# Optimization experiments

Measured on AMD Instinct MI355X. Metric: run time of the kernel, lower is better.

## Reference

```python
import jax, jax.numpy as jnp
import numpy as np
import math

DIM = 1024
CHUNK = 64
B, S = 4, 4096

def setup_inputs() -> dict:
    key = jax.random.key(0)
    ks = jax.random.split(key, 16)
    d = DIM
    std = 1.0 / math.sqrt(d)
    def lin(k):
        k1, k2 = jax.random.split(k)
        return (jax.random.uniform(k1, (d, d), jnp.float32, -std, std),
                jax.random.uniform(k2, (d,), jnp.float32, -std, std))
    Wk, bk = lin(ks[0])
    Wv, bv = lin(ks[1])
    Wq, bq = lin(ks[2])
    Wkp, bkp = lin(ks[3])
    Wqp, bqp = lin(ks[4])
    Wo, bo = lin(ks[5])
    return {
        "x": jax.random.normal(ks[6], (B, S, d), jnp.float32),
        "Wk": Wk, "bk": bk, "Wv": Wv, "bv": bv, "Wq": Wq, "bq": bq,
        "Wkp": Wkp, "bkp": bkp, "Wqp": Wqp, "bqp": bqp,
        "phase_scale": jnp.full((d,), math.pi, jnp.float32),
        "ln_g": jnp.ones((d,), jnp.float32),
        "ln_b": jnp.zeros((d,), jnp.float32),
        "Wo": Wo, "bo": bo,
    }

def _linear(x, W, b):
    # torch nn.Linear: x @ W.T + b
    return jnp.einsum('bsd,ed->bse', x, W) + b

def _layernorm(x, g, b, eps=1e-5):
    mu = jnp.mean(x, axis=-1, keepdims=True)
    var = jnp.var(x, axis=-1, keepdims=True)
    return (x - mu) * jax.lax.rsqrt(var + eps) * g + b

def reference(x, Wk, bk, Wv, bv, Wq, bq, Wkp, bkp, Wqp, bqp,
              phase_scale, ln_g, ln_b, Wo, bo):
    batch, seq_len, dim = x.shape
    key = _linear(x, Wk, bk)
    value = _linear(x, Wv, bv)
    query = _linear(x, Wq, bq)
    key_phase = jnp.tanh(_linear(key, Wkp, bkp)) * phase_scale
    query_phase = jnp.tanh(_linear(query, Wqp, bqp)) * phase_scale
    bound_real = value * jnp.cos(key_phase)
    bound_imag = value * jnpp_sin(key_phase) if False else value * jnp.sin(key_phase)
    pad_len = (CHUNK - seq_len % CHUNK) % CHUNK
    if pad_len > 0:
        pad = ((0, 0), (0, pad_len), (0, 0))
        bound_real = jnp.pad(bound_real, pad)
        bound_imag = jnp.pad(bound_imag, pad)
        query_phase = jnp.pad(query_phase, pad)
    padded_len = bound_real.shape[1]
    nc = padded_len // CHUNK
    br = bound_real.reshape(batch, nc, CHUNK, dim)
    bi = bound_imag.reshape(batch, nc, CHUNK, dim)
    qp = query_phase.reshape(batch, nc, CHUNK, dim)
    mem_real = jnp.cumsum(br, axis=2)
    mem_imag = jnp.cumsum(bi, axis=2)
    retrieved = mem_real * jnp.cos(qp) + mem_imag * jnp.sin(qp)
    retrieved = retrieved.reshape(batch, padded_len, dim)[:, :seq_len]
    retrieved = retrieved / math.sqrt(dim)
    out = _linear(_layernorm(retrieved, ln_g, ln_b), Wo, bo)
    return x + out
```

## Files before the change

kernel.cpp:

```cpp
#include <hip/hip_runtime.h>
#include <math.h>

#define DIMD 1024
#define CHUNKLEN 64
#define NTOK 16384

#define TM 128
#define TN 128
#define BK 64

typedef __bf16 bf16x8 __attribute__((ext_vector_type(8)));
typedef float floatx4 __attribute__((ext_vector_type(4)));
typedef unsigned short ushort8v __attribute__((ext_vector_type(8)));

__device__ __forceinline__ float bf2f(unsigned short u) {
  union { unsigned int i; float f; } v; v.i = ((unsigned int)u) << 16; return v.f;
}
__device__ __forceinline__ unsigned short f2bf(float f) {
  union { float f; unsigned int i; } v; v.f = f;
  unsigned int r = v.i + 0x7FFFu + ((v.i >> 16) & 1u);
  return (unsigned short)(r >> 16);
}

__device__ __forceinline__ float tanh_fast(float v) {
  const float t = __expf(2.0f * v);
  return 1.0f - 2.0f * __builtin_amdgcn_rcpf(t + 1.0f);
}

__device__ __forceinline__ void async16(const unsigned short* g, unsigned short* l) {
  __builtin_amdgcn_global_load_lds(
      (const __attribute__((address_space(1))) unsigned int*)g,
      (__attribute__((address_space(3))) unsigned int*)l, 16, 0, 0);
}

__global__ __launch_bounds__(256) void cvt_all_kernel(
    const float* __restrict__ x,
    const float* __restrict__ w0, const float* __restrict__ w1,
    const float* __restrict__ w2, const float* __restrict__ w3,
    unsigned short* __restrict__ dx,
    unsigned short* __restrict__ d0, unsigned short* __restrict__ d1,
    unsigned short* __restrict__ d2, unsigned short* __restrict__ d3)
{
  const int b = blockIdx.x;
  const float* src; unsigned short* dst; long i;
  if (b < 16384) {
    src = x; dst = dx; i = (long)b * 256 + threadIdx.x;
  } else {
    const int r = b - 16384;
    const int s = r >> 10;
    src = s == 0 ? w0 : s == 1 ? w1 : s == 2 ? w2 : w3;
    dst = s == 0 ? d0 : s == 1 ? d1 : s == 2 ? d2 : d3;
    i = (long)(r & 1023) * 256 + threadIdx.x;
  }
  const float4 v = ((const float4*)src)[i];
  ushort4 o;
  o.x = f2bf(v.x); o.y = f2bf(v.y); o.z = f2bf(v.z); o.w = f2bf(v.w);
  ((ushort4*)dst)[i] = o;
}

__global__ __launch_bounds__(256) void transpose_cvt_kernel(
    const float* __restrict__ s0, const float* __restrict__ s1,
    unsigned short* __restrict__ q0, unsigned short* __restrict__ q1)
{
  __shared__ unsigned short tile[64][66];
  const float* src = blockIdx.z ? s1 : s0;
  unsigned short* dst = blockIdx.z ? q1 : q0;
  const int e0 = blockIdx.y * 64;
  const int k0 = blockIdx.x * 64;
  const int t  = threadIdx.x;
  const int tr = t >> 4;
  const int tc = t & 15;
#pragma unroll
  for (int p = 0; p < 4; ++p) {
    const int el = p * 16 + tr;
    const float4 v = *(const float4*)&src[(long)(e0 + el) * DIMD + k0 + tc * 4];
    tile[el][tc * 4 + 0] = f2bf(v.x);
    tile[el][tc * 4 + 1] = f2bf(v.y);
    tile[el][tc * 4 + 2] = f2bf(v.z);
    tile[el][tc * 4 + 3] = f2bf(v.w);
  }
  __syncthreads();
#pragma unroll
  for (int p = 0; p < 4; ++p) {
    const int kl = p * 16 + tr;
    ushort4 o;
    o.x = tile[tc * 4 + 0][kl];
    o.y = tile[tc * 4 + 1][kl];
    o.z = tile[tc * 4 + 2][kl];
    o.w = tile[tc * 4 + 3][kl];
    *(ushort4*)&dst[(long)(k0 + kl) * DIMD + e0 + tc * 4] = o;
  }
}

__global__ __launch_bounds__(256) void bias_comb_kernel(
    const float* __restrict__ Wkp, const float* __restrict__ bk,
    const float* __restrict__ bkp,
    const float* __restrict__ Wqp, const float* __restrict__ bq,
    const float* __restrict__ bqp,
    float* __restrict__ bkq, float* __restrict__ bqq)
{
  const int b = blockIdx.x;
  const int which = b >> 8;
  const int lane = threadIdx.x & 63;
  const int wid  = threadIdx.x >> 6;
  const int n = (b & 255) * 4 + wid;
  const float* W    = which ? Wqp : Wkp;
  const float* bvec = which ? bq  : bk;
  const float* badd = which ? bqp : bkp;
  float*       outp = which ? bqq : bkq;
  float s = 0.f;
#pragma unroll
  for (int i = 0; i < 16; ++i)
    s += W[(long)n * DIMD + lane + i * 64] * bvec[lane + i * 64];
#pragma unroll
  for (int o = 32; o > 0; o >>= 1) s += __shfl_xor(s, o, 64);
  if (lane == 0) outp[n] = s + badd[n];
}

template <int MODE>
__global__ __launch_bounds__(256) void gemm_bt_kernel(
    const unsigned short* __restrict__ A0, const unsigned short* __restrict__ A1,
    const unsigned short* __restrict__ W0, const unsigned short* __restrict__ W1,
    const unsigned short* __restrict__ W2,
    const float* __restrict__ b0, const float* __restrict__ b1,
    const float* __restrict__ b2,
    const float* __restrict__ aux,
    unsigned short* __restrict__ O0, unsigned short* __restrict__ O1,
    unsigned short* __restrict__ O2,
    float* __restrict__ Of, const float* __restrict__ resid)
{
  __shared__ unsigned short lsA[TM * BK];
  __shared__ unsigned short lsB[TN * BK];

  const int tid  = threadIdx.x;
  const int lane = tid & 63;
  const int wid  = tid >> 6;
  const long bm  = (long)blockIdx.y * TM;
  const long bng = (long)blockIdx.x * TN;

  const unsigned short* A = A0;
  const unsigned short* W = W0;
  const float* bias = b0;
  unsigned short* Ob = O0;
  long bn = bng;
  int seg = 0;
  if (MODE == 0) {
    seg = (int)(bng >> 10);
    bn = bng & 1023;
    W    = seg == 0 ? W0 : (seg == 1 ? W1 : W2);
    bias = seg == 0 ? b0 : (seg == 1 ? b1 : b2);
    Ob   = seg == 0 ? O0 : (seg == 1 ? O1 : O2);
  } else if (MODE == 1) {
    if (blockIdx.z) { A = A1; W = W1; Ob = O1; }
  }

  const int wm = (wid & 1) * 64;
  const int wn = (wid >> 1) * 64;

  floatx4 acc[4][4];
#pragma unroll
  for (int i = 0; i < 4; ++i)
#pragma unroll
    for (int j = 0; j < 4; ++j)
      acc[i][j] = (floatx4)(0.0f);

  const int srow  = lane >> 3;
  const int pcol  = (lane & 7) * 8;
  const int lcolL = (((lane & 7) ^ (srow & 7)) * 8);
  const int frm   = lane & 15;
  const int cfrk  = lane >> 4;

  for (int kk = 0; kk < DIMD; kk += BK) {
    __syncthreads();
#pragma unroll
    for (int j = 0; j < 4; ++j) {
      const int inst = wid * 4 + j;
      const int r = inst * 8 + srow;
      async16(A + (bm + r) * (long)DIMD + kk + lcolL, &lsA[r * BK + pcol]);
      async16(W + (bn + r) * (long)DIMD + kk + lcolL, &lsB[r * BK + pcol]);
    }
    __syncthreads();
#pragma unroll
    for (int ks = 0; ks < BK; ks += 32) {
      const int cb  = (ks >> 3) + cfrk;
      const int swz = ((cb ^ (frm & 7)) << 3);
      bf16x8 af[4], bfr[4];
#pragma unroll
      for (int i = 0; i < 4; ++i)
        af[i]  = *(const bf16x8*)&lsA[(wm + i * 16 + frm) * BK + swz];
#pragma unroll
      for (int i = 0; i < 4; ++i)
        bfr[i] = *(const bf16x8*)&lsB[(wn + i * 16 + frm) * BK + swz];
#pragma unroll
      for (int i = 0; i < 4; ++i)
#pragma unroll
        for (int j = 0; j < 4; ++j)
          acc[i][j] = __builtin_amdgcn_mfma_f32_16x16x32_bf16(af[i], bfr[j], acc[i][j], 0, 0, 0);
    }
  }

  const int cn = lane & 15;
  const int rq = (lane >> 4) * 4;
#pragma unroll
  for (int j = 0; j < 4; ++j) {
    const long col = bn + wn + j * 16 + cn;
    const float bv = (MODE == 1) ? 0.0f : bias[col];
    const float pv = (MODE == 0) ? aux[col] : 0.0f;
#pragma unroll
    for (int i = 0; i < 4; ++i) {
#pragma unroll
      for (int r = 0; r < 4; ++r) {
        const long row = bm + wm + i * 16 + rq + r;
        const float v = acc[i][j][r] + bv;
        if (MODE == 0) {
          Ob[row * (long)DIMD + col] = (seg == 0) ? f2bf(v)
                                                  : f2bf(tanh_fast(v) * pv);
        } else if (MODE == 1) {
          Ob[row * (long)DIMD + col] = f2bf(v);
        } else {
          Of[row * (long)DIMD + col] = v + resid[row * (long)DIMD + col];
        }
      }
    }
  }
}

#define TILE16 16384
#define HALF16 8192

template <int MODE>
__global__ __launch_bounds__(512, 2) void gemm256_kernel(
    const unsigned short* __restrict__ A,
    const unsigned short* __restrict__ W0, const unsigned short* __restrict__ W1,
    const unsigned short* __restrict__ W2,
    const float* __restrict__ b0, const float* __restrict__ b1,
    const float* __restrict__ b2,
    const float* __restrict__ aux,
    unsigned short* __restrict__ O0, unsigned short* __restrict__ O1,
    unsigned short* __restrict__ O2,
    float* __restrict__ Of, const float* __restrict__ resid)
{
  __shared__ unsigned short lds[4 * TILE16];

  const int tid  = threadIdx.x;
  const int lane = tid & 63;
  const int wid  = tid >> 6;

  constexpr int NBX = (MODE == 0) ? 12 : 4;
  constexpr int NWG = NBX * 64;
  const int orig = blockIdx.x + blockIdx.y * gridDim.x;
  const int swzb = (orig & 7) * (NWG >> 3) + (orig >> 3);
  const int nb = swzb % NBX;
  const int mb = swzb / NBX;

  const long bm = (long)mb * 256;
  long bn;
  int seg = 0;
  const unsigned short* W = W0;
  const float* bias = b0;
  unsigned short* Ob = O0;
  if (MODE == 0) {
    seg = nb >> 2;
    bn  = (long)(nb & 3) * 256;
    W    = seg == 0 ? W0 : (seg == 1 ? W1 : W2);
    bias = seg == 0 ? b0 : (seg == 1 ? b1 : b2);
    Ob   = seg == 0 ? O0 : (seg == 1 ? O1 : O2);
  } else {
    bn = (long)nb * 256;
  }

  const int wm = (wid >> 2) * 128;
  const int wn = (wid & 3) * 64;

  const int q0  = wid * 2;
  const int sr0 = q0 * 16 + (lane >> 2);
  const int sg  = (((lane & 3) ^ ((sr0 >> 1) & 3)) * 8);
  const int sd0 = q0 * 512 + lane * 8;
  const long arow = (bm + sr0) * (long)DIMD;
  const long brow = (bn + sr0) * (long)DIMD;

  const int frm   = lane & 15;
  const int cfrk  = lane >> 4;
  const int slot8 = (cfrk ^ ((frm >> 1) & 3)) * 8;
  const int rbase = frm * 32 + slot8;

  floatx4 acc[8][4];
#pragma unroll
  for (int i = 0; i < 8; ++i)
#pragma unroll
    for (int j = 0; j < 4; ++j) acc[i][j] = (floatx4)(0.0f);

  bf16x8 bfr[4];

#define SA256(buf, kk, h) do { \
    const unsigned short* _s = A + arow + (kk) + (h) * 32 + sg; \
    unsigned short* _d = &lds[(buf) * TILE16 + (h) * HALF16 + sd0]; \
    async16(_s, _d); \
    async16(_s + 16 * DIMD, _d + 512); \
  } while (0)
#define SB256(buf, kk, h) do { \
    const unsigned short* _s = W + brow + (kk) + (h) * 32 + sg; \
    unsigned short* _d = &lds[2 * TILE16 + (buf) * TILE16 + (h) * HALF16 + sd0]; \
    async16(_s, _d); \
    async16(_s + 16 * DIMD, _d + 512); \
  } while (0)
#define RDA256(buf, h, ih, af) do { \
    const int _ab = (buf) * TILE16 + (h) * HALF16 + (wm + (ih) * 64) * 32 + rbase; \
    _Pragma("unroll") \
    for (int _i = 0; _i < 4; ++_i) (af)[_i] = *(const bf16x8*)&lds[_ab + _i * 512]; \
  } while (0)
#define RDB256(buf, h) do { \
    const int _bb = 2 * TILE16 + (buf) * TILE16 + (h) * HALF16 + wn * 32 + rbase; \
    _Pragma("unroll") \
    for (int _j = 0; _j < 4; ++_j) bfr[_j] = *(const bf16x8*)&lds[_bb + _j * 512]; \
  } while (0)
#define VMW4() asm volatile("s_waitcnt vmcnt(4)" ::: "memory")
#define BAR256() do { \
    asm volatile("" ::: "memory"); \
    __builtin_amdgcn_s_barrier(); \
    asm volatile("" ::: "memory"); \
  } while (0)
#define MFMA16(ih, af) do { \
    __builtin_amdgcn_s_setprio(1); \
    _Pragma("unroll") \
    for (int _i = 0; _i < 4; ++_i) \
      _Pragma("unroll") \
      for (int _j = 0; _j < 4; ++_j) \
        acc[(ih) * 4 + _i][_j] = __builtin_amdgcn_mfma_f32_16x16x32_bf16( \
            (af)[_i], bfr[_j], acc[(ih) * 4 + _i][_j], 0, 0, 0); \
    __builtin_amdgcn_s_setprio(0); \
  } while (0)
#define KTILE(c, n, kn) do { \
    { bf16x8 af[4]; RDA256(c, 0, 0, af); RDB256(c, 0); \
      SA256(n, kn, 0); MFMA16(0, af); } \
    { bf16x8 af[4]; RDA256(c, 0, 1, af); \
      SB256(n, kn, 0); VMW4(); BAR256(); MFMA16(1, af); } \
    { bf16x8 af[4]; RDA256(c, 1, 0, af); RDB256(c, 1); \
      SA256(n, kn, 1); MFMA16(0, af); } \
    { bf16x8 af[4]; RDA256(c, 1, 1, af); \
      SB256(n, kn, 1); VMW4(); BAR256(); MFMA16(1, af); } \
  } while (0)

  SA256(0, 0, 0); SB256(0, 0, 0); SA256(0, 0, 1); SB256(0, 0, 1);
  VMW4();
  BAR256();

#pragma unroll 1
  for (int t = 0; t < 16; t += 2) {
    const int k1 = (t + 1) * 64;
    const int k2 = (t + 2 < 16) ? (t + 2) * 64 : 0;
    KTILE(0, 1, k1);
    KTILE(1, 0, k2);
  }
  asm volatile("s_waitcnt vmcnt(0)" ::: "memory");

#undef SA256
#undef SB256
#undef RDA256
#undef RDB256
#undef VMW4
#undef BAR256
#undef MFMA16
#undef KTILE

  const int cn = lane & 15;
  const int rq = (lane >> 4) * 4;
  long colj[4]; float bvj[4], pvj[4];
#pragma unroll
  for (int j = 0; j < 4; ++j) {
    colj[j] = bn + wn + j * 16 + cn;
    bvj[j]  = bias[colj[j]];
    pvj[j]  = (MODE == 0) ? aux[colj[j]] : 0.0f;
  }
#pragma unroll
  for (int ii = 0; ii < 8; ++ii) {
#pragma unroll
    for (int r = 0; r < 4; ++r) {
      const long rowo = (bm + wm + ii * 16 + rq + r) * (long)DIMD;
#pragma unroll
      for (int j = 0; j < 4; ++j) {
        const float v = acc[ii][j][r] + bvj[j];
        if (MODE == 0) {
          Ob[rowo + colj[j]] = (seg == 0) ? f2bf(v)
                                          : f2bf(tanh_fast(v) * pvj[j]);
        } else {
          Of[rowo + colj[j]] = v + resid[rowo + colj[j]];
        }
      }
    }
  }
}

__global__ __launch_bounds__(512) void scan_ln_kernel(
    const unsigned short* __restrict__ V,  const unsigned short* __restrict__ KP,
    const unsigned short* __restrict__ QP,
    const float* __restrict__ lng, const float* __restrict__ lnb,
    unsigned short* __restrict__ out)
{
  __shared__ unsigned short ret_s[32][DIMD];

  const int tid  = threadIdx.x;
  const int lane = tid & 63;
  const int wid  = tid >> 6;
  const long rowBase = (long)blockIdx.x * CHUNKLEN;
  const int d0 = tid * 2;

  const int c0 = lane * 8;
  const int c1 = 512 + lane * 8;
  float g0[8], be0[8], g1[8], be1[8];
#pragma unroll
  for (int j = 0; j < 8; ++j) {
    g0[j] = lng[c0 + j]; be0[j] = lnb[c0 + j];
    g1[j] = lng[c1 + j]; be1[j] = lnb[c1 + j];
  }

  float mr[2] = {0.f, 0.f};
  float mi[2] = {0.f, 0.f};

  for (int h = 0; h < 2; ++h) {
    for (int tl = 0; tl < 32; ++tl) {
      const int t = h * 32 + tl;
      const long off = (rowBase + t) * DIMD + d0;
      const ushort2 v2 = *(const ushort2*)(V + off);
      const ushort2 k2 = *(const ushort2*)(KP + off);
      const ushort2 q2 = *(const ushort2*)(QP + off);
      const unsigned short va[2] = {v2.x, v2.y};
      const unsigned short ka[2] = {k2.x, k2.y};
      const unsigned short qa[2] = {q2.x, q2.y};
      unsigned short rv[2];
#pragma unroll
      for (int j = 0; j < 2; ++j) {
        const float v  = bf2f(va[j]);
        const float kp = bf2f(ka[j]);
        const float qp = bf2f(qa[j]);
        float skp, ckp, sqp, cqp;
        __sincosf(kp, &skp, &ckp);
        __sincosf(qp, &sqp, &cqp);
        mr[j] += v * ckp;
        mi[j] += v * skp;
        rv[j] = f2bf((mr[j] * cqp + mi[j] * sqp) * 0.03125f);
      }
      ushort2 o2; o2.x = rv[0]; o2.y = rv[1];
      *(ushort2*)&ret_s[tl][d0] = o2;
    }
    __syncthreads();

#pragma unroll 1
    for (int rr = 0; rr < 4; ++rr) {
      const int tl = wid * 4 + rr;
      const ushort8v a0 = *(const ushort8v*)&ret_s[tl][c0];
      const ushort8v a1 = *(const ushort8v*)&ret_s[tl][c1];
      float f0[8], f1[8];
      float s = 0.f, s2 = 0.f;
#pragma unroll
      for (int j = 0; j < 8; ++j) {
        f0[j] = bf2f(a0[j]); f1[j] = bf2f(a1[j]);
        s += f0[j] + f1[j];
        s2 += f0[j] * f0[j] + f1[j] * f1[j];
      }
#pragma unroll
      for (int o = 32; o > 0; o >>= 1) {
        s  += __shfl_xor(s,  o, 64);
        s2 += __shfl_xor(s2, o, 64);
      }
      const float mu  = s * (1.0f / DIMD);
      const float var = s2 * (1.0f / DIMD) - mu * mu;
      const float inv = rsqrtf(var + 1e-5f);
      ushort8v o0, o1;
#pragma unroll
      for (int j = 0; j < 8; ++j) {
        o0[j] = f2bf((f0[j] - mu) * inv * g0[j] + be0[j]);
        o1[j] = f2bf((f1[j] - mu) * inv * g1[j] + be1[j]);
      }
      const long gro = (rowBase + h * 32 + tl) * DIMD;
      *(ushort8v*)(out + gro + c0) = o0;
      *(ushort8v*)(out + gro + c1) = o1;
    }
    __syncthreads();
  }
}

extern "C" void kernel_launch(void* const* d_in, const int* in_sizes, int n_in,
                              void* d_out, int out_size, void* d_ws, size_t ws_size,
                              hipStream_t stream)
{
  const float* x   = (const float*)d_in[0];
  const float* Wk  = (const float*)d_in[1];
  const float* bk  = (const float*)d_in[2];
  const float* Wv  = (const float*)d_in[3];
  const float* bv  = (const float*)d_in[4];
  const float* Wq  = (const float*)d_in[5];
  const float* bq  = (const float*)d_in[6];
  const float* Wkp = (const float*)d_in[7];
  const float* bkp = (const float*)d_in[8];
  const float* Wqp = (const float*)d_in[9];
  const float* bqp = (const float*)d_in[10];
  const float* ph  = (const float*)d_in[11];
  const float* lng = (const float*)d_in[12];
  const float* lnb = (const float*)d_in[13];
  const float* Wo  = (const float*)d_in[14];
  const float* bo  = (const float*)d_in[15];
  float* out = (float*)d_out;

  const long NB = (long)NTOK * DIMD;
  const long DD = (long)DIMD * DIMD;
  const size_t required = (size_t)(4 * NB + 8 * DD) * sizeof(unsigned short)
                        + 2048 * sizeof(float);
  if (ws_size < required) return;

  unsigned short* S0   = (unsigned short*)d_ws;
  unsigned short* SV   = S0   + NB;
  unsigned short* SKP  = SV   + NB;
  unsigned short* SQP  = SKP  + NB;
  unsigned short* Wvb  = SQP  + NB;
  unsigned short* Wob  = Wvb  + DD;
  unsigned short* Wkpb = Wob  + DD;
  unsigned short* Wqpb = Wkpb + DD;
  unsigned short* WkT  = Wqpb + DD;
  unsigned short* WqT  = WkT  + DD;
  unsigned short* Wkqb = WqT  + DD;
  unsigned short* Wqqb = Wkqb + DD;
  float* bkq = (float*)(Wqqb + DD);
  float* bqq = bkq + DIMD;

  dim3 blk(256);

  cvt_all_kernel<<<dim3(16384 + 4 * 1024), blk, 0, stream>>>(
      x, Wv, Wo, Wkp, Wqp, S0, Wvb, Wob, Wkpb, Wqpb);
  transpose_cvt_kernel<<<dim3(16, 16, 2), blk, 0, stream>>>(Wk, Wq, WkT, WqT);
  bias_comb_kernel<<<dim3(512), blk, 0, stream>>>(Wkp, bk, bkp, Wqp, bq, bqp, bkq, bqq);
  gemm_bt_kernel<1><<<dim3(DIMD / TN, DIMD / TM, 2), blk, 0, stream>>>(
      Wkpb, Wqpb, WkT, WqT, nullptr, nullptr, nullptr, nullptr, nullptr,
      Wkqb, Wqqb, nullptr, nullptr, nullptr);
  gemm256_kernel<0><<<dim3(12, NTOK / 256), dim3(512), 0, stream>>>(
      S0, Wvb, Wkqb, Wqqb, bv, bkq, bqq, ph, SV, SKP, SQP, nullptr, nullptr);
  scan_ln_kernel<<<dim3(NTOK / CHUNKLEN), dim3(512), 0, stream>>>(
      SV, SKP, SQP, lng, lnb, S0);
  gemm256_kernel<2><<<dim3(4, NTOK / 256), dim3(512), 0, stream>>>(
      S0, Wob, nullptr, nullptr, bo, nullptr, nullptr, nullptr,
      nullptr, nullptr, nullptr, out, x);
}
```

Baseline: 358.9 us.

## Merge prep kernels, split QKV GEMM, use hardware sin/cos on pre-scaled phases

Folds the weight-conversion, transpose and bias-combine kernels into a single prep launch to cut launch overhead. Splits the fused 12-tile projection GEMM into a V GEMM and a separate key/query-phase GEMM. The phase GEMM now stores phases pre-multiplied by 1/(2π), so the scan can call the native amdgcn sin/cos instructions (which take turns, not radians) instead of __sincosf. The scan loop is also unrolled by 4. The split adds one extra launch and may reduce occupancy in each GEMM, in exchange for cheaper transcendental work in the scan.

```diff
diff --git a/kernel.cpp b/kernel.cpp
--- a/kernel.cpp
+++ b/kernel.cpp
@@ -8,6 +8,8 @@
 #define TM 128
 #define TN 128
 #define BK 64
+
+#define INV2PI 0.15915494309189535f
 
 typedef __bf16 bf16x8 __attribute__((ext_vector_type(8)));
 typedef float floatx4 __attribute__((ext_vector_type(4)));
@@ -33,101 +35,92 @@
       (__attribute__((address_space(3))) unsigned int*)l, 16, 0, 0);
 }
 
-__global__ __launch_bounds__(256) void cvt_all_kernel(
+__global__ __launch_bounds__(256) void prep_kernel(
     const float* __restrict__ x,
     const float* __restrict__ w0, const float* __restrict__ w1,
     const float* __restrict__ w2, const float* __restrict__ w3,
     unsigned short* __restrict__ dx,
     unsigned short* __restrict__ d0, unsigned short* __restrict__ d1,
-    unsigned short* __restrict__ d2, unsigned short* __restrict__ d3)
-{
-  const int b = blockIdx.x;
-  const float* src; unsigned short* dst; long i;
-  if (b < 16384) {
-    src = x; dst = dx; i = (long)b * 256 + threadIdx.x;
-  } else {
-    const int r = b - 16384;
-    const int s = r >> 10;
-    src = s == 0 ? w0 : s == 1 ? w1 : s == 2 ? w2 : w3;
-    dst = s == 0 ? d0 : s == 1 ? d1 : s == 2 ? d2 : d3;
-    i = (long)(r & 1023) * 256 + threadIdx.x;
-  }
-  const float4 v = ((const float4*)src)[i];
-  ushort4 o;
-  o.x = f2bf(v.x); o.y = f2bf(v.y); o.z = f2bf(v.z); o.w = f2bf(v.w);
-  ((ushort4*)dst)[i] = o;
-}
-
-__global__ __launch_bounds__(256) void transpose_cvt_kernel(
-    const float* __restrict__ s0, const float* __restrict__ s1,
-    unsigned short* __restrict__ q0, unsigned short* __restrict__ q1)
-{
-  __shared__ unsigned short tile[64][66];
-  const float* src = blockIdx.z ? s1 : s0;
-  unsigned short* dst = blockIdx.z ? q1 : q0;
-  const int e0 = blockIdx.y * 64;
-  const int k0 = blockIdx.x * 64;
-  const int t  = threadIdx.x;
-  const int tr = t >> 4;
-  const int tc = t & 15;
-#pragma unroll
-  for (int p = 0; p < 4; ++p) {
-    const int el = p * 16 + tr;
-    const float4 v = *(const float4*)&src[(long)(e0 + el) * DIMD + k0 + tc * 4];
-    tile[el][tc * 4 + 0] = f2bf(v.x);
-    tile[el][tc * 4 + 1] = f2bf(v.y);
-    tile[el][tc * 4 + 2] = f2bf(v.z);
-    tile[el][tc * 4 + 3] = f2bf(v.w);
-  }
-  __syncthreads();
-#pragma unroll
-  for (int p = 0; p < 4; ++p) {
-    const int kl = p * 16 + tr;
-    ushort4 o;
-    o.x = tile[tc * 4 + 0][kl];
-    o.y = tile[tc * 4 + 1][kl];
-    o.z = tile[tc * 4 + 2][kl];
-    o.w = tile[tc * 4 + 3][kl];
-    *(ushort4*)&dst[(long)(k0 + kl) * DIMD + e0 + tc * 4] = o;
-  }
-}
-
-__global__ __launch_bounds__(256) void bias_comb_kernel(
-    const float* __restrict__ Wkp, const float* __restrict__ bk,
-    const float* __restrict__ bkp,
-    const float* __restrict__ Wqp, const float* __restrict__ bq,
-    const float* __restrict__ bqp,
+    unsigned short* __restrict__ d2, unsigned short* __restrict__ d3,
+    const float* __restrict__ Wk, const float* __restrict__ Wq,
+    unsigned short* __restrict__ WkT, unsigned short* __restrict__ WqT,
+    const float* __restrict__ bk, const float* __restrict__ bkp,
+    const float* __restrict__ bq, const float* __restrict__ bqp,
     float* __restrict__ bkq, float* __restrict__ bqq)
 {
   const int b = blockIdx.x;
-  const int which = b >> 8;
-  const int lane = threadIdx.x & 63;
-  const int wid  = threadIdx.x >> 6;
-  const int n = (b & 255) * 4 + wid;
-  const float* W    = which ? Wqp : Wkp;
-  const float* bvec = which ? bq  : bk;
-  const float* badd = which ? bqp : bkp;
-  float*       outp = which ? bqq : bkq;
-  float s = 0.f;
-#pragma unroll
-  for (int i = 0; i < 16; ++i)
-    s += W[(long)n * DIMD + lane + i * 64] * bvec[lane + i * 64];
-#pragma unroll
-  for (int o = 32; o > 0; o >>= 1) s += __shfl_xor(s, o, 64);
-  if (lane == 0) outp[n] = s + badd[n];
+  if (b < 20480) {
+    const float* src; unsigned short* dst; long i;
+    if (b < 16384) {
+      src = x; dst = dx; i = (long)b * 256 + threadIdx.x;
+    } else {
+      const int r = b - 16384;
+      const int s = r >> 10;
+      src = s == 0 ? w0 : s == 1 ? w1 : s == 2 ? w2 : w3;
+      dst = s == 0 ? d0 : s == 1 ? d1 : s == 2 ? d2 : d3;
+      i = (long)(r & 1023) * 256 + threadIdx.x;
+    }
+    const float4 v = ((const float4*)src)[i];
+    ushort4 o;
+    o.x = f2bf(v.x); o.y = f2bf(v.y); o.z = f2bf(v.z); o.w = f2bf(v.w);
+    ((ushort4*)dst)[i] = o;
+  } else if (b < 20992) {
+    __shared__ unsigned short tile[64][66];
+    const int r2 = b - 20480;
+    const int z  = r2 >> 8;
+    const int rem = r2 & 255;
+    const float* src = z ? Wq : Wk;
+    unsigned short* dst = z ? WqT : WkT;
+    const int k0 = (rem & 15) * 64;
+    const int e0 = (rem >> 4) * 64;
+    const int t  = threadIdx.x;
+    const int tr = t >> 4;
+    const int tc = t & 15;
+#pragma unroll
+    for (int p = 0; p < 4; ++p) {
+      const int el = p * 16 + tr;
+      const float4 v = *(const float4*)&src[(long)(e0 + el) * DIMD + k0 + tc * 4];
+      tile[el][tc * 4 + 0] = f2bf(v.x);
+      tile[el][tc * 4 + 1] = f2bf(v.y);
+      tile[el][tc * 4 + 2] = f2bf(v.z);
+      tile[el][tc * 4 + 3] = f2bf(v.w);
+    }
+    __syncthreads();
+#pragma unroll
+    for (int p = 0; p < 4; ++p) {
+      const int kl = p * 16 + tr;
+      ushort4 o;
+      o.x = tile[tc * 4 + 0][kl];
+      o.y = tile[tc * 4 + 1][kl];
+      o.z = tile[tc * 4 + 2][kl];
+      o.w = tile[tc * 4 + 3][kl];
+      *(ushort4*)&dst[(long)(k0 + kl) * DIMD + e0 + tc * 4] = o;
+    }
+  } else {
+    const int r3 = b - 20992;
+    const int which = r3 >> 8;
+    const int lane = threadIdx.x & 63;
+    const int wid  = threadIdx.x >> 6;
+    const int n = (r3 & 255) * 4 + wid;
+    const float* W    = which ? w3 : w2;
+    const float* bvec = which ? bq  : bk;
+    const float* badd = which ? bqp : bkp;
+    float*       outp = which ? bqq : bkq;
+    float s = 0.f;
+#pragma unroll
+    for (int i = 0; i < 16; ++i)
+      s += W[(long)n * DIMD + lane + i * 64] * bvec[lane + i * 64];
+#pragma unroll
+    for (int o = 32; o > 0; o >>= 1) s += __shfl_xor(s, o, 64);
+    if (lane == 0) outp[n] = s + badd[n];
+  }
 }
 
 template <int MODE>
 __global__ __launch_bounds__(256) void gemm_bt_kernel(
     const unsigned short* __restrict__ A0, const unsigned short* __restrict__ A1,
     const unsigned short* __restrict__ W0, const unsigned short* __restrict__ W1,
-    const unsigned short* __restrict__ W2,
-    const float* __restrict__ b0, const float* __restrict__ b1,
-    const float* __restrict__ b2,
-    const float* __restrict__ aux,
-    unsigned short* __restrict__ O0, unsigned short* __restrict__ O1,
-    unsigned short* __restrict__ O2,
-    float* __restrict__ Of, const float* __restrict__ resid)
+    unsigned short* __restrict__ O0, unsigned short* __restrict__ O1)
 {
   __shared__ unsigned short lsA[TM * BK];
   __shared__ unsigned short lsB[TN * BK];
@@ -136,23 +129,12 @@
   const int lane = tid & 63;
   const int wid  = tid >> 6;
   const long bm  = (long)blockIdx.y * TM;
-  const long bng = (long)blockIdx.x * TN;
+  const long bn  = (long)blockIdx.x * TN;
 
   const unsigned short* A = A0;
   const unsigned short* W = W0;
-  const float* bias = b0;
   unsigned short* Ob = O0;
-  long bn = bng;
-  int seg = 0;
-  if (MODE == 0) {
-    seg = (int)(bng >> 10);
-    bn = bng & 1023;
-    W    = seg == 0 ? W0 : (seg == 1 ? W1 : W2);
-    bias = seg == 0 ? b0 : (seg == 1 ? b1 : b2);
-    Ob   = seg == 0 ? O0 : (seg == 1 ? O1 : O2);
-  } else if (MODE == 1) {
-    if (blockIdx.z) { A = A1; W = W1; Ob = O1; }
-  }
+  if (blockIdx.z) { A = A1; W = W1; Ob = O1; }
 
   const int wm = (wid & 1) * 64;
   const int wn = (wid >> 1) * 64;
@@ -204,22 +186,12 @@
 #pragma unroll
   for (int j = 0; j < 4; ++j) {
     const long col = bn + wn + j * 16 + cn;
-    const float bv = (MODE == 1) ? 0.0f : bias[col];
-    const float pv = (MODE == 0) ? aux[col] : 0.0f;
 #pragma unroll
     for (int i = 0; i < 4; ++i) {
 #pragma unroll
       for (int r = 0; r < 4; ++r) {
         const long row = bm + wm + i * 16 + rq + r;
-        const float v = acc[i][j][r] + bv;
-        if (MODE == 0) {
-          Ob[row * (long)DIMD + col] = (seg == 0) ? f2bf(v)
-                                                  : f2bf(tanh_fast(v) * pv);
-        } else if (MODE == 1) {
-          Ob[row * (long)DIMD + col] = f2bf(v);
-        } else {
-          Of[row * (long)DIMD + col] = v + resid[row * (long)DIMD + col];
-        }
+        Ob[row * (long)DIMD + col] = f2bf(acc[i][j][r]);
       }
     }
   }
@@ -246,7 +218,7 @@
   const int lane = tid & 63;
   const int wid  = tid >> 6;
 
-  constexpr int NBX = (MODE == 0) ? 12 : 4;
+  constexpr int NBX = (MODE == 3) ? 8 : 4;
   constexpr int NWG = NBX * 64;
   const int orig = blockIdx.x + blockIdx.y * gridDim.x;
   const int swzb = (orig & 7) * (NWG >> 3) + (orig >> 3);
@@ -255,16 +227,15 @@
 
   const long bm = (long)mb * 256;
   long bn;
-  int seg = 0;
   const unsigned short* W = W0;
   const float* bias = b0;
   unsigned short* Ob = O0;
-  if (MODE == 0) {
-    seg = nb >> 2;
-    bn  = (long)(nb & 3) * 256;
-    W    = seg == 0 ? W0 : (seg == 1 ? W1 : W2);
-    bias = seg == 0 ? b0 : (seg == 1 ? b1 : b2);
-    Ob   = seg == 0 ? O0 : (seg == 1 ? O1 : O2);
+  if (MODE == 3) {
+    const int sl = nb >> 2;
+    bn   = (long)(nb & 3) * 256;
+    W    = sl ? W2 : W1;
+    bias = sl ? b2 : b1;
+    Ob   = sl ? O2 : O1;
   } else {
     bn = (long)nb * 256;
   }
@@ -370,7 +341,7 @@
   for (int j = 0; j < 4; ++j) {
     colj[j] = bn + wn + j * 16 + cn;
     bvj[j]  = bias[colj[j]];
-    pvj[j]  = (MODE == 0) ? aux[colj[j]] : 0.0f;
+    pvj[j]  = (MODE == 3) ? aux[colj[j]] * INV2PI : 0.0f;
   }
 #pragma unroll
   for (int ii = 0; ii < 8; ++ii) {
@@ -381,8 +352,9 @@
       for (int j = 0; j < 4; ++j) {
         const float v = acc[ii][j][r] + bvj[j];
         if (MODE == 0) {
-          Ob[rowo + colj[j]] = (seg == 0) ? f2bf(v)
-                                          : f2bf(tanh_fast(v) * pvj[j]);
+          Ob[rowo + colj[j]] = f2bf(v);
+        } else if (MODE == 3) {
+          Ob[rowo + colj[j]] = f2bf(tanh_fast(v) * pvj[j]);
         } else {
           Of[rowo + colj[j]] = v + resid[rowo + colj[j]];
         }
@@ -418,6 +390,7 @@
   float mi[2] = {0.f, 0.f};
 
   for (int h = 0; h < 2; ++h) {
+#pragma unroll 4
     for (int tl = 0; tl < 32; ++tl) {
       const int t = h * 32 + tl;
       const long off = (rowBase + t) * DIMD + d0;
@@ -433,9 +406,10 @@
         const float v  = bf2f(va[j]);
         const float kp = bf2f(ka[j]);
         const float qp = bf2f(qa[j]);
-        float skp, ckp, sqp, cqp;
-        __sincosf(kp, &skp, &ckp);
-        __sincosf(qp, &sqp, &cqp);
+        const float skp = __builtin_amdgcn_sinf(kp);
+        const float ckp = __builtin_amdgcn_cosf(kp);
+        const float sqp = __builtin_amdgcn_sinf(qp);
+        const float cqp = __builtin_amdgcn_cosf(qp);
         mr[j] += v * ckp;
         mi[j] += v * skp;
         rv[j] = f2bf((mr[j] * cqp + mi[j] * sqp) * 0.03125f);
@@ -523,17 +497,17 @@
   float* bkq = (float*)(Wqqb + DD);
   float* bqq = bkq + DIMD;
 
-  dim3 blk(256);
-
-  cvt_all_kernel<<<dim3(16384 + 4 * 1024), blk, 0, stream>>>(
-      x, Wv, Wo, Wkp, Wqp, S0, Wvb, Wob, Wkpb, Wqpb);
-  transpose_cvt_kernel<<<dim3(16, 16, 2), blk, 0, stream>>>(Wk, Wq, WkT, WqT);
-  bias_comb_kernel<<<dim3(512), blk, 0, stream>>>(Wkp, bk, bkp, Wqp, bq, bqp, bkq, bqq);
-  gemm_bt_kernel<1><<<dim3(DIMD / TN, DIMD / TM, 2), blk, 0, stream>>>(
-      Wkpb, Wqpb, WkT, WqT, nullptr, nullptr, nullptr, nullptr, nullptr,
-      Wkqb, Wqqb, nullptr, nullptr, nullptr);
-  gemm256_kernel<0><<<dim3(12, NTOK / 256), dim3(512), 0, stream>>>(
-      S0, Wvb, Wkqb, Wqqb, bv, bkq, bqq, ph, SV, SKP, SQP, nullptr, nullptr);
+  prep_kernel<<<dim3(16384 + 4 * 1024 + 512 + 512), dim3(256), 0, stream>>>(
+      x, Wv, Wo, Wkp, Wqp, S0, Wvb, Wob, Wkpb, Wqpb,
+      Wk, Wq, WkT, WqT, bk, bkp, bq, bqp, bkq, bqq);
+  gemm_bt_kernel<1><<<dim3(DIMD / TN, DIMD / TM, 2), dim3(256), 0, stream>>>(
+      Wkpb, Wqpb, WkT, WqT, Wkqb, Wqqb);
+  gemm256_kernel<0><<<dim3(4, NTOK / 256), dim3(512), 0, stream>>>(
+      S0, Wvb, nullptr, nullptr, bv, nullptr, nullptr, nullptr,
+      SV, nullptr, nullptr, nullptr, nullptr);
+  gemm256_kernel<3><<<dim3(8, NTOK / 256), dim3(512), 0, stream>>>(
+      S0, nullptr, Wkqb, Wqqb, nullptr, bkq, bqq, ph,
+      nullptr, SKP, SQP, nullptr, nullptr);
   scan_ln_kernel<<<dim3(NTOK / CHUNKLEN), dim3(512), 0, stream>>>(
       SV, SKP, SQP, lng, lnb, S0);
   gemm256_kernel<2><<<dim3(4, NTOK / 256), dim3(512), 0, stream>>>(
```

Result: no change. 354.3 us (-1.3%).
